# Kernel tuning notes

Measured on AMD Instinct MI355X. Metric: run time of the kernel, lower is better.

The kernel has to match this reference:

```python
import jax, jax.numpy as jnp
import numpy as np

E = 512       # token_size
H = 8         # num_heads
DH = E // H   # head dim
S = 16        # sequence_len (steps)
B = 128       # batch
MAX_SEQ = 64  # max_seq_len
IN = 256      # input_size
OUT = 128     # output_sz
NL = 2        # num_layers
MEM = E * MAX_SEQ + 1  # memory_size (last slot stores cur_idx)
EPS = 1e-5
NEG = -1e9


def _ln(x, s, b):
    mu = x.mean(-1, keepdims=True)
    var = ((x - mu) ** 2).mean(-1, keepdims=True)
    return (x - mu) / jnp.sqrt(var + EPS) * s + b


def _mha(x, mask, w_in, b_in, w_out, b_out):
    # x: (B, L, E); mask: (B, 1, L, L) bool, True = masked (torch semantics)
    bsz, L, _ = x.shape
    qkv = x @ w_in.T + b_in                      # (B, L, 3E)
    q, k, v = jnp.split(qkv, 3, axis=-1)
    q = q.reshape(bsz, L, H, DH)
    k = k.reshape(bsz, L, H, DH)
    v = v.reshape(bsz, L, H, DH)
    scores = jnp.einsum('bqhd,bkhd->bhqk', q, k) / jnp.sqrt(jnp.asarray(DH, x.dtype))
    scores = jnp.where(mask, NEG, scores)
    attn = jax.nn.softmax(scores, axis=-1)
    out = jnp.einsum('bhqk,bkhd->bqhd', attn, v).reshape(bsz, L, E)
    return out @ w_out.T + b_out


def setup_inputs() -> dict:
    key = jax.random.key(0)
    ks = jax.random.split(key, 16)
    sc = 0.02
    return {
        'sequences': jax.random.normal(ks[0], (S, B, IN), jnp.float32),
        'h_state': jnp.zeros((1, B, MEM), jnp.float32),
        'Win': jax.random.normal(ks[1], (E, IN), jnp.float32) * sc,
        'b_in': jnp.zeros((E,), jnp.float32),
        'Wout': jax.random.normal(ks[2], (OUT, E), jnp.float32) * sc,
        'b_out': jnp.zeros((OUT,), jnp.float32),
        'in_proj_w': jax.random.normal(ks[3], (NL, 3 * E, E), jnp.float32) * sc,
        'in_proj_b': jnp.zeros((NL, 3 * E), jnp.float32),
        'attn_out_w': jax.random.normal(ks[4], (NL, E, E), jnp.float32) * sc,
        'attn_out_b': jnp.zeros((NL, E), jnp.float32),
        'ln1_scale': jnp.ones((NL, E), jnp.float32),
        'ln1_bias': jnp.zeros((NL, E), jnp.float32),
        'ln2_scale': jnp.ones((NL, E), jnp.float32),
        'ln2_bias': jnp.zeros((NL, E), jnp.float32),
        'ff_w': jax.random.normal(ks[5], (NL, E, E), jnp.float32) * sc,
        'ff_b': jnp.zeros((NL, E), jnp.float32),
    }


def reference(sequences, h_state, Win, b_in, Wout, b_out, in_proj_w, in_proj_b,
              attn_out_w, attn_out_b, ln1_scale, ln1_bias, ln2_scale, ln2_bias,
              ff_w, ff_b):
    x = sequences @ Win.T + b_in                 # (S, B, E)
    h0 = h_state[0]
    cur_idx = h0[:, -1].astype(jnp.int32)        # (B,), zeros at rollout start
    hbuf = h0[:, :-1].reshape(B, MAX_SEQ, E)
    # fresh memory (cur_idx == 0) => max_len_here = S, static
    pad = hbuf[:, S:, :]
    h = hbuf[:, :S, :]
    pos = jnp.arange(S)
    bidx = jnp.arange(B)

    def step(carry, x_t):
        h, ci = carry
        h = h.at[bidx, ci].set(x_t)              # slot scatter write
        invalid = pos[None, :] > ci[:, None]     # (B, S)
        mask = invalid[:, None, :] | invalid[:, :, None]
        mask = mask & (pos != 0)[None, None, :]  # column 0 always attendable
        mask = mask[:, None, :, :]               # broadcast over heads
        for l in range(NL):
            attn = _mha(h, mask, in_proj_w[l], in_proj_b[l], attn_out_w[l], attn_out_b[l])
            h = _ln(h + attn, ln1_scale[l], ln1_bias[l])
            h = _ln(h + h @ ff_w[l].T + ff_b[l], ln2_scale[l], ln2_bias[l])
        out = h[bidx, ci] @ Wout.T + b_out       # (B, OUT)
        return (h, ci + 1), out

    (h_fin, ci_fin), outputs = jax.lax.scan(step, (h, cur_idx), x)
    new_h = jnp.concatenate([h_fin, pad], axis=1).reshape(B, MEM - 1)
    new_h = jnp.concatenate([new_h, ci_fin[:, None].astype(new_h.dtype)], axis=-1)[None]
    return outputs, new_h
```

## Files before the change

kernel.cpp:

```cpp
#include <hip/hip_runtime.h>

typedef __attribute__((ext_vector_type(8))) short short8;
typedef __attribute__((ext_vector_type(4))) float f32x4;
typedef __attribute__((ext_vector_type(4))) int int4v;
typedef unsigned short ushort_t;
typedef unsigned char u8;

#define E 512
#define SS 16
#define BB 128
#define IND 256
#define OUTD 128
#define MEMD 32769
#define NEGV -1000000000.0f
#define EPSV 1e-5f

#define MFMA  __builtin_amdgcn_mfma_f32_16x16x32_bf16
#define MFMAI8(a, b, c) __builtin_amdgcn_mfma_i32_16x16x64_i8((a), (b), (c), 0, 0, 0)

#define GLV(dst, base, off) \
  asm volatile("global_load_dwordx4 %0, %1, %2" : "=v"(dst) : "v"(off), "s"(base))
#define WVX_(x, n) asm volatile("s_waitcnt vmcnt(" #n ")" : "+v"(x))
#define WVX(x, n) WVX_(x, n)

__device__ __forceinline__ void bar_lds() {
  asm volatile("s_waitcnt lgkmcnt(0)\ns_barrier" ::: "memory");
}

__device__ __forceinline__ unsigned short f2bf(float f) {
  union { float f; unsigned int u; } v; v.f = f;
  unsigned int u = v.u;
  unsigned int r = u + 0x7fffu + ((u >> 16) & 1u);
  return (unsigned short)(r >> 16);
}
__device__ __forceinline__ float bf2f(unsigned short h) {
  union { unsigned int u; float f; } v; v.u = ((unsigned int)h) << 16;
  return v.f;
}
__device__ __forceinline__ int q8(float x) {
  return __float2int_rn(fminf(fmaxf(x, -127.f), 127.f));
}
__device__ __forceinline__ void quant8_store(u8* dst, const float* h) {
  int q[8];
#pragma unroll
  for (int j = 0; j < 8; ++j) q[j] = q8(h[j] * 32.f);
  unsigned int p0 = (q[0]&255) | ((q[1]&255)<<8) | ((q[2]&255)<<16) | ((q[3]&255)<<24);
  unsigned int p1 = (q[4]&255) | ((q[5]&255)<<8) | ((q[6]&255)<<16) | ((q[7]&255)<<24);
  *(unsigned int*)(dst)     = p0;
  *(unsigned int*)(dst + 4) = p1;
}

__global__ __launch_bounds__(256) void wscale_kernel(
    const float* __restrict__ ipw, const float* __restrict__ aow,
    const float* __restrict__ ffw, const float* __restrict__ wout,
    float* __restrict__ scl)
{
  int wv = blockIdx.x * 4 + (threadIdx.x >> 6);
  int lane = threadIdx.x & 63;
  const float* row;
  if (wv < 3072)      row = ipw  + (size_t)wv * 512;
  else if (wv < 4096) row = aow  + (size_t)(wv - 3072) * 512;
  else if (wv < 5120) row = ffw  + (size_t)(wv - 4096) * 512;
  else                row = wout + (size_t)(wv - 5120) * 512;
  float m = 0.f;
#pragma unroll
  for (int k = 0; k < 8; ++k) m = fmaxf(m, fabsf(row[lane + 64*k]));
  m = fmaxf(m, __shfl_xor(m, 1));
  m = fmaxf(m, __shfl_xor(m, 2));
  m = fmaxf(m, __shfl_xor(m, 4));
  m = fmaxf(m, __shfl_xor(m, 8));
  m = fmaxf(m, __shfl_xor(m, 16));
  m = fmaxf(m, __shfl_xor(m, 32));
  if (lane == 0) scl[wv] = (m > 0.f) ? m * (1.f / 127.f) : 1.f;
}

__device__ __forceinline__ void packmatI8(u8* __restrict__ dst, const float* __restrict__ src,
                                          const float* __restrict__ sclrow,
                                          int n, int tid, int stride) {
  for (int i = tid; i < n; i += stride) {
    int j = i & 15, lane = (i >> 4) & 63, kt = (i >> 10) & 7, T = i >> 13;
    int row = T * 16 + (lane & 15);
    int col = kt * 64 + ((lane >> 4) << 4) + j;
    float s = sclrow[row];
    int q = q8(src[(size_t)row * 512 + col] / s);
    dst[i] = (u8)(q & 0xff);
  }
}

__global__ __launch_bounds__(256) void wconvert_kernel(
    const float* __restrict__ ipw, const float* __restrict__ aow,
    const float* __restrict__ ffw, const float* __restrict__ wout,
    const float* __restrict__ win, const float* __restrict__ scl,
    u8* __restrict__ win8, u8* __restrict__ wo8,
    u8* __restrict__ wf8, u8* __restrict__ wout8,
    float* __restrict__ winT)
{
  const int tid = blockIdx.x * blockDim.x + threadIdx.x;
  const int stride = gridDim.x * blockDim.x;
  packmatI8(win8,  ipw,  scl,        2*1536*E, tid, stride);
  packmatI8(wo8,   aow,  scl + 3072, 2*E*E,    tid, stride);
  packmatI8(wf8,   ffw,  scl + 4096, 2*E*E,    tid, stride);
  packmatI8(wout8, wout, scl + 5120, OUTD*E,   tid, stride);
  for (int i = tid; i < E*IND; i += stride) {
    int o = i / IND, k = i % IND;
    winT[k*E + o] = win[i];
  }
}

__global__ __launch_bounds__(512) void xproj_kernel(
    const float* __restrict__ seq, const float* __restrict__ winT,
    const float* __restrict__ b_in, float* __restrict__ X)
{
  const int b = blockIdx.x;
  const int th = threadIdx.x;
  __shared__ float sq[SS * IND];
  for (int i = th; i < SS * IND; i += 512) {
    int t = i >> 8, k = i & 255;
    sq[i] = seq[((size_t)t * BB + b) * IND + k];
  }
  __syncthreads();
  float acc[SS];
#pragma unroll
  for (int t = 0; t < SS; ++t) acc[t] = 0.f;
  for (int k = 0; k < IND; ++k) {
    float w = winT[k * E + th];
#pragma unroll
    for (int t = 0; t < SS; ++t) acc[t] += sq[t * IND + k] * w;
  }
  float bias = b_in[th];
#pragma unroll
  for (int t = 0; t < SS; ++t)
    X[((size_t)t * BB + b) * E + th] = acc[t] + bias;
}

__global__ __launch_bounds__(1024, 4) void encoder_kernel(
    const float* __restrict__ Xpre, const float* __restrict__ hstate,
    const u8* __restrict__ win8, const u8* __restrict__ wo8,
    const u8* __restrict__ wf8, const u8* __restrict__ wout8,
    const float* __restrict__ scl,
    const float* __restrict__ ipb, const float* __restrict__ aob,
    const float* __restrict__ l1s, const float* __restrict__ l1b,
    const float* __restrict__ l2s, const float* __restrict__ l2b,
    const float* __restrict__ ffb, const float* __restrict__ bout,
    float* __restrict__ out)
{
  const int b = blockIdx.x;
  const int th = threadIdx.x;
  const int lane = th & 63;
  const int w = th >> 6;
  const int g = lane >> 4;
  const int c = lane & 15;
  const int fb = lane << 3;
  const int fq = w*16 + c;

  unsigned int vofs[8];
#pragma unroll
  for (int i = 0; i < 8; ++i)
    vofs[i] = (unsigned int)w * 8192u + (unsigned int)lane * 16u + (unsigned int)i * 1024u;

  __shared__ u8 h_i8[16*528];
  __shared__ ushort_t qk[9216];
  __shared__ ushort_t vbuf[10240];
  __shared__ ushort_t p_lds[2560];
  __shared__ ushort_t lnp[4096];

  ushort_t* q_lds = qk;
  ushort_t* k_lds = qk + 4608;
  u8* abuf_i8 = (u8*)qk;
  ushort_t* dbuf = qk;

  const size_t hsb = (size_t)b * MEMD;
  const int ci0 = (int)hstate[hsb + 32768];
  const float boutr = bout[(w&7)*16 + c];
  const float mw = scl[5120 + (w&7)*16 + c] * (1.f/32.f);

  float hreg[8];
  {
#pragma unroll
    for (int j = 0; j < 8; ++j) hreg[j] = hstate[hsb + (size_t)w*E + fb + j];
    quant8_store(h_i8 + w*528 + fb, hreg);
  }
  for (int i = th; i < 2560; i += 1024) p_lds[i] = 0;
  for (int i = th; i < 4096; i += 1024) {
    int h2 = i >> 10, dh = (i >> 4) & 63, t16 = i & 15;
    vbuf[h2*2560 + dh*40 + 16 + t16] = 0;
  }
  for (int i = th; i < 4096; i += 1024) {
    int l = i >> 11, arr = (i >> 9) & 3, idx = i & 511;
    float v = (arr == 0 ? l1s : arr == 1 ? l1b : arr == 2 ? l2s : l2b)[l*512 + idx];
    lnp[i] = f2bf(v);
  }
  bar_lds();

#pragma unroll 1
  for (int t = 0; t < SS; ++t) {
    const int cic = ci0 + t;
    if (cic < 16 && w == cic) {
#pragma unroll
      for (int j = 0; j < 8; ++j) hreg[j] = Xpre[((size_t)t*BB + b)*E + fb + j];
      quant8_store(h_i8 + w*528 + fb, hreg);
    }
    bar_lds();

#pragma unroll 1
    for (int l = 0; l < 2; ++l) {
      const float* bq_ = ipb + l*1536 + fq;
      const float biq0 = bq_[0],    biq1 = bq_[256];
      const float bik0 = bq_[512],  bik1 = bq_[768];
      const float biv0 = bq_[1024], biv1 = bq_[1280];
      const float aob0 = aob[l*512 + fq], aob1 = aob[l*512 + 256 + fq];
      const float ffb0 = ffb[l*512 + fq], ffb1 = ffb[l*512 + 256 + fq];
      const float* sip = scl + l*1536;
      const float mq0 = sip[fq]       * (1.f/32.f), mq1 = sip[256 + fq]  * (1.f/32.f);
      const float mk0 = sip[512 + fq] * (1.f/32.f), mk1 = sip[768 + fq]  * (1.f/32.f);
      const float mv0 = sip[1024+ fq] * (1.f/32.f), mv1 = sip[1280 + fq] * (1.f/32.f);
      const float* swo = scl + 3072 + l*512;
      const float mo0 = swo[fq] * (1.f/32.f), mo1 = swo[256 + fq] * (1.f/32.f);
      const float* swf = scl + 4096 + l*512;
      const float mf0 = swf[fq] * (1.f/32.f), mf1 = swf[256 + fq] * (1.f/32.f);

      const u8* wiL = win8 + (size_t)l*786432;
      const u8* woL = wo8 + (size_t)l*262144;
      const u8* wfL = wf8 + (size_t)l*262144;

      int4v oacc0 = {0,0,0,0}, oacc1 = oacc0;

#pragma unroll 1
      for (int pass = 0; pass < 2; ++pass) {
        const int hl = w >> 2;
        const int dhb = (w & 3) * 16;

        {
          const u8* A8 = h_i8 + c*528 + g*16;
          const u8* uq = wiL + (size_t)pass*131072;
          const u8* uk = uq + 262144;
          const u8* uv = uq + 524288;
          int4v aq = {0,0,0,0}, ak = aq, av = aq;
          int4v Bq[4], Bk[4], Bv[4];
          GLV(Bq[0], uq, vofs[0]); GLV(Bk[0], uk, vofs[0]); GLV(Bv[0], uv, vofs[0]);
          GLV(Bq[1], uq, vofs[1]); GLV(Bk[1], uk, vofs[1]); GLV(Bv[1], uv, vofs[1]);
          GLV(Bq[2], uq, vofs[2]); GLV(Bk[2], uk, vofs[2]); GLV(Bv[2], uv, vofs[2]);
          GLV(Bq[3], uq, vofs[3]); GLV(Bk[3], uk, vofs[3]); GLV(Bv[3], uv, vofs[3]);

#define QKV_STEP(kt2, nq, nk, nv) { \
            int4v a = *(const int4v*)(A8 + (kt2)*64); \
            WVX(Bq[(kt2)&3], nq); aq = MFMAI8(a, Bq[(kt2)&3], aq); \
            WVX(Bk[(kt2)&3], nk); ak = MFMAI8(a, Bk[(kt2)&3], ak); \
            WVX(Bv[(kt2)&3], nv); av = MFMAI8(a, Bv[(kt2)&3], av); \
            if ((kt2) < 4) { \
              GLV(Bq[(kt2)&3], uq, vofs[(kt2)+4]); \
              GLV(Bk[(kt2)&3], uk, vofs[(kt2)+4]); \
              GLV(Bv[(kt2)&3], uv, vofs[(kt2)+4]); \
            } }
          QKV_STEP(0, 11, 10, 9)
          QKV_STEP(1, 11, 10, 9)
          QKV_STEP(2, 11, 10, 9)
          QKV_STEP(3, 11, 10, 9)
          QKV_STEP(4, 11, 10, 9)
          QKV_STEP(5,  8,  7, 6)
          QKV_STEP(6,  5,  4, 3)
          QKV_STEP(7,  2,  1, 0)

          const float biq = pass ? biq1 : biq0;
          const float bik = pass ? bik1 : bik0;
          const float biv = pass ? biv1 : biv0;
          const float mq = pass ? mq1 : mq0;
          const float mk = pass ? mk1 : mk0;
          const float mv = pass ? mv1 : mv0;
#pragma unroll
          for (int r = 0; r < 4; ++r) {
            int tok = 4*g + r;
            q_lds[hl*1152 + tok*72 + dhb + c] = f2bf((float)aq[r]*mq + biq);
            k_lds[hl*1152 + tok*72 + dhb + c] = f2bf((float)ak[r]*mk + bik);
            vbuf[hl*2560 + (dhb + c)*40 + tok] = f2bf((float)av[r]*mv + biv);
          }
        }
        bar_lds();

        int4v O0[4], O1[4];
        {
          const u8* uo0 = woL + pass*4096;
          const u8* uo1 = uo0 + 131072;
          GLV(O0[0], uo0, vofs[0]); GLV(O1[0], uo1, vofs[0]);
          GLV(O0[1], uo0, vofs[1]); GLV(O1[1], uo1, vofs[1]);
          GLV(O0[2], uo0, vofs[2]); GLV(O1[2], uo1, vofs[2]);
          GLV(O0[3], uo0, vofs[3]); GLV(O1[3], uo1, vofs[3]);
        }

        if (w < 4) {
          f32x4 sc = {0.f,0.f,0.f,0.f};
#pragma unroll
          for (int k2 = 0; k2 < 2; ++k2) {
            short8 qa = *(const short8*)&q_lds[w*1152 + c*72 + k2*32 + g*8];
            short8 kb = *(const short8*)&k_lds[w*1152 + c*72 + k2*32 + g*8];
            sc = MFMA(qa, kb, sc, 0,0,0);
          }
          float sv[4], mx[4], ex[4], sm[4];
#pragma unroll
          for (int r = 0; r < 4; ++r) {
            int row = 4*g + r;
            bool msk = ((c > cic) || (row > cic)) && (c != 0);
            sv[r] = msk ? NEGV : sc[r]*0.125f;
            mx[r] = sv[r];
          }
#pragma unroll
          for (int r = 0; r < 4; ++r) {
            mx[r] = fmaxf(mx[r], __shfl_xor(mx[r], 1));
            mx[r] = fmaxf(mx[r], __shfl_xor(mx[r], 2));
            mx[r] = fmaxf(mx[r], __shfl_xor(mx[r], 4));
            mx[r] = fmaxf(mx[r], __shfl_xor(mx[r], 8));
          }
#pragma unroll
          for (int r = 0; r < 4; ++r) { ex[r] = __expf(sv[r] - mx[r]); sm[r] = ex[r]; }
#pragma unroll
          for (int r = 0; r < 4; ++r) {
            sm[r] += __shfl_xor(sm[r], 1);
            sm[r] += __shfl_xor(sm[r], 2);
            sm[r] += __shfl_xor(sm[r], 4);
            sm[r] += __shfl_xor(sm[r], 8);
          }
#pragma unroll
          for (int r = 0; r < 4; ++r)
            p_lds[w*640 + (4*g + r)*40 + c] = f2bf(ex[r] / sm[r]);
        }
        bar_lds();

        {
          const int hl2 = w >> 2, ct = w & 3;
          short8 pa = *(const short8*)&p_lds[hl2*640 + c*40 + g*8];
          short8 vb = *(const short8*)&vbuf[hl2*2560 + (ct*16 + c)*40 + g*8];
          f32x4 ov = {0.f,0.f,0.f,0.f};
          ov = MFMA(pa, vb, ov, 0,0,0);
#pragma unroll
          for (int r = 0; r < 4; ++r)
            abuf_i8[(4*g + r)*272 + hl2*64 + ct*16 + c] = (u8)(q8(ov[r]*32.f) & 0xff);
        }
        bar_lds();

        {
          const u8* A8o = abuf_i8 + c*272 + g*16;
#define OP_STEP(kt2, n0, n1) { \
            int4v a = *(const int4v*)(A8o + (kt2)*64); \
            WVX(O0[kt2], n0); oacc0 = MFMAI8(a, O0[kt2], oacc0); \
            WVX(O1[kt2], n1); oacc1 = MFMAI8(a, O1[kt2], oacc1); }
          OP_STEP(0, 7, 6)
          OP_STEP(1, 5, 4)
          OP_STEP(2, 3, 2)
          OP_STEP(3, 1, 0)
        }
        bar_lds();
      }

#pragma unroll
      for (int r = 0; r < 4; ++r) {
        dbuf[(4*g + r)*520 + fq]       = f2bf((float)oacc0[r]*mo0 + aob0);
        dbuf[(4*g + r)*520 + 256 + fq] = f2bf((float)oacc1[r]*mo1 + aob1);
      }
      bar_lds();

      int4v F0[4], F1[4];
      const u8* uf0 = wfL;
      const u8* uf1 = wfL + 131072;
      GLV(F0[0], uf0, vofs[0]); GLV(F1[0], uf1, vofs[0]);
      GLV(F0[1], uf0, vofs[1]); GLV(F1[1], uf1, vofs[1]);
      GLV(F0[2], uf0, vofs[2]); GLV(F1[2], uf1, vofs[2]);
      GLV(F0[3], uf0, vofs[3]); GLV(F1[3], uf1, vofs[3]);

      {
        const ushort_t* lpS = lnp + l*2048;
        const ushort_t* lpB = lnp + l*2048 + 512;
        float sum = 0.f;
#pragma unroll
        for (int j = 0; j < 8; ++j) {
          hreg[j] += bf2f(dbuf[w*520 + fb + j]);
          sum += hreg[j];
        }
        sum += __shfl_xor(sum, 1); sum += __shfl_xor(sum, 2); sum += __shfl_xor(sum, 4);
        sum += __shfl_xor(sum, 8); sum += __shfl_xor(sum, 16); sum += __shfl_xor(sum, 32);
        float mu = sum * (1.0f/512.0f);
        float s2 = 0.f;
#pragma unroll
        for (int j = 0; j < 8; ++j) { float dd = hreg[j] - mu; s2 += dd*dd; }
        s2 += __shfl_xor(s2, 1); s2 += __shfl_xor(s2, 2); s2 += __shfl_xor(s2, 4);
        s2 += __shfl_xor(s2, 8); s2 += __shfl_xor(s2, 16); s2 += __shfl_xor(s2, 32);
        float rs = rsqrtf(s2 * (1.0f/512.0f) + EPSV);
#pragma unroll
        for (int j = 0; j < 8; ++j)
          hreg[j] = (hreg[j] - mu) * rs * bf2f(lpS[fb + j]) + bf2f(lpB[fb + j]);
        quant8_store(h_i8 + w*528 + fb, hreg);
      }
      bar_lds();

      {
        int4v f0 = {0,0,0,0}, f1 = f0;
        const u8* A8 = h_i8 + c*528 + g*16;
#define FF_STEP(kt2, n0, n1) { \
          int4v a = *(const int4v*)(A8 + (kt2)*64); \
          WVX(F0[(kt2)&3], n0); f0 = MFMAI8(a, F0[(kt2)&3], f0); \
          WVX(F1[(kt2)&3], n1); f1 = MFMAI8(a, F1[(kt2)&3], f1); \
          if ((kt2) < 4) { \
            GLV(F0[(kt2)&3], uf0, vofs[(kt2)+4]); \
            GLV(F1[(kt2)&3], uf1, vofs[(kt2)+4]); \
          } }
        FF_STEP(0, 7, 6)
        FF_STEP(1, 7, 6)
        FF_STEP(2, 7, 6)
        FF_STEP(3, 7, 6)
        FF_STEP(4, 7, 6)
        FF_STEP(5, 5, 4)
        FF_STEP(6, 3, 2)
        FF_STEP(7, 1, 0)
        bar_lds();
#pragma unroll
        for (int r = 0; r < 4; ++r) {
          dbuf[(4*g + r)*520 + fq]       = f2bf((float)f0[r]*mf0 + ffb0);
          dbuf[(4*g + r)*520 + 256 + fq] = f2bf((float)f1[r]*mf1 + ffb1);
        }
      }
      bar_lds();

      {
        const ushort_t* lpS = lnp + l*2048 + 1024;
        const ushort_t* lpB = lnp + l*2048 + 1536;
        float sum = 0.f;
#pragma unroll
        for (int j = 0; j < 8; ++j) {
          hreg[j] += bf2f(dbuf[w*520 + fb + j]);
          sum += hreg[j];
        }
        sum += __shfl_xor(sum, 1); sum += __shfl_xor(sum, 2); sum += __shfl_xor(sum, 4);
        sum += __shfl_xor(sum, 8); sum += __shfl_xor(sum, 16); sum += __shfl_xor(sum, 32);
        float mu = sum * (1.0f/512.0f);
        float s2 = 0.f;
#pragma unroll
        for (int j = 0; j < 8; ++j) { float dd = hreg[j] - mu; s2 += dd*dd; }
        s2 += __shfl_xor(s2, 1); s2 += __shfl_xor(s2, 2); s2 += __shfl_xor(s2, 4);
        s2 += __shfl_xor(s2, 8); s2 += __shfl_xor(s2, 16); s2 += __shfl_xor(s2, 32);
        float rs = rsqrtf(s2 * (1.0f/512.0f) + EPSV);
#pragma unroll
        for (int j = 0; j < 8; ++j)
          hreg[j] = (hreg[j] - mu) * rs * bf2f(lpS[fb + j]) + bf2f(lpB[fb + j]);
        quant8_store(h_i8 + w*528 + fb, hreg);
      }
      bar_lds();
    }

    if (w < 8) {
      const int crow = (cic < 15) ? cic : 15;
      const u8* A8 = h_i8 + c*528 + g*16;
      int4v WB[8];
      GLV(WB[0], wout8, vofs[0]); GLV(WB[1], wout8, vofs[1]);
      GLV(WB[2], wout8, vofs[2]); GLV(WB[3], wout8, vofs[3]);
      GLV(WB[4], wout8, vofs[4]); GLV(WB[5], wout8, vofs[5]);
      GLV(WB[6], wout8, vofs[6]); GLV(WB[7], wout8, vofs[7]);
      int4v oo = {0,0,0,0};
#define WOUT_STEP(kt2, n) { \
        int4v a = *(const int4v*)(A8 + (kt2)*64); \
        WVX(WB[kt2], n); oo = MFMAI8(a, WB[kt2], oo); }
      WOUT_STEP(0, 7)
      WOUT_STEP(1, 6)
      WOUT_STEP(2, 5)
      WOUT_STEP(3, 4)
      WOUT_STEP(4, 3)
      WOUT_STEP(5, 2)
      WOUT_STEP(6, 1)
      WOUT_STEP(7, 0)
      if (g == (crow >> 2)) {
        int r = crow & 3;
        int val = (r == 0) ? oo[0] : (r == 1) ? oo[1] : (r == 2) ? oo[2] : oo[3];
        out[((size_t)t*BB + b)*OUTD + w*16 + c] = (float)val * mw + boutr;
      }
    }
    bar_lds();
  }

  const size_t OB = (size_t)SS * BB * OUTD;
#pragma unroll
  for (int j = 0; j < 8; ++j)
    out[OB + hsb + (size_t)w*E + fb + j] = hreg[j];
  for (int i = th; i < 48*512; i += 1024)
    out[OB + hsb + 8192 + i] = hstate[hsb + 8192 + i];
  if (th == 0) out[OB + hsb + 32768] = (float)(ci0 + SS);
}

extern "C" void kernel_launch(void* const* d_in, const int* in_sizes, int n_in,
                              void* d_out, int out_size, void* d_ws, size_t ws_size,
                              hipStream_t stream) {
  const float* seq  = (const float*)d_in[0];
  const float* hs   = (const float*)d_in[1];
  const float* Win  = (const float*)d_in[2];
  const float* b_in = (const float*)d_in[3];
  const float* Wout = (const float*)d_in[4];
  const float* bo   = (const float*)d_in[5];
  const float* ipw  = (const float*)d_in[6];
  const float* ipb  = (const float*)d_in[7];
  const float* aow  = (const float*)d_in[8];
  const float* aob  = (const float*)d_in[9];
  const float* l1s  = (const float*)d_in[10];
  const float* l1b  = (const float*)d_in[11];
  const float* l2s  = (const float*)d_in[12];
  const float* l2b  = (const float*)d_in[13];
  const float* ffw  = (const float*)d_in[14];
  const float* ffb  = (const float*)d_in[15];

  char* ws = (char*)d_ws;
  u8*    win8  = (u8*)   (ws + 0);
  u8*    wo8   = (u8*)   (ws + 1572864);
  u8*    wf8   = (u8*)   (ws + 2097152);
  u8*    wout8 = (u8*)   (ws + 2621440);
  float* scl   = (float*)(ws + 2686976);
  float* winT  = (float*)(ws + 2707968);
  float* X     = (float*)(ws + 3232256);

  wscale_kernel<<<1312, 256, 0, stream>>>(ipw, aow, ffw, Wout, scl);
  wconvert_kernel<<<512, 256, 0, stream>>>(ipw, aow, ffw, Wout, Win, scl,
                                           win8, wo8, wf8, wout8, winT);
  xproj_kernel<<<BB, 512, 0, stream>>>(seq, winT, b_in, X);
  encoder_kernel<<<BB, 1024, 0, stream>>>(X, hs, win8, wo8, wf8, wout8, scl,
                                          ipb, aob, l1s, l1b, l2s, l2b, ffb, bo,
                                          (float*)d_out);
}
```

Baseline: 785.3 us.

## Prefetch next QKV weight tiles across phases and fuse softmax with PV per wave

Hoists the first two QKV weight tile loads out of each pass, issuing them during the previous phase (after the out-projection, after the layer norm, after the output projection), so they overlap with earlier work and the stall at the start of each QKV GEMM shrinks. It also has all 16 waves compute the score and softmax tile redundantly into a private per-wave P buffer. That lets each wave feed its own PV MFMA directly, removing one block-wide barrier per pass. The cost is extra LDS (a larger P buffer and a separate attention-output buffer) and duplicated QK/softmax work. The vmcnt wait counts inside the existing macros must stay consistent with the loads now issued earlier.

```diff
diff --git a/kernel.cpp b/kernel.cpp
--- a/kernel.cpp
+++ b/kernel.cpp
@@ -161,12 +161,12 @@
   __shared__ u8 h_i8[16*528];
   __shared__ ushort_t qk[9216];
   __shared__ ushort_t vbuf[10240];
-  __shared__ ushort_t p_lds[2560];
+  __shared__ ushort_t p_w[9216];
+  __shared__ u8 abuf_i8[16*272];
   __shared__ ushort_t lnp[4096];
 
   ushort_t* q_lds = qk;
   ushort_t* k_lds = qk + 4608;
-  u8* abuf_i8 = (u8*)qk;
   ushort_t* dbuf = qk;
 
   const size_t hsb = (size_t)b * MEMD;
@@ -180,7 +180,7 @@
     for (int j = 0; j < 8; ++j) hreg[j] = hstate[hsb + (size_t)w*E + fb + j];
     quant8_store(h_i8 + w*528 + fb, hreg);
   }
-  for (int i = th; i < 2560; i += 1024) p_lds[i] = 0;
+  for (int i = th; i < 9216; i += 1024) p_w[i] = 0;
   for (int i = th; i < 4096; i += 1024) {
     int h2 = i >> 10, dh = (i >> 4) & 63, t16 = i & 15;
     vbuf[h2*2560 + dh*40 + 16 + t16] = 0;
@@ -191,6 +191,14 @@
     lnp[i] = f2bf(v);
   }
   bar_lds();
+
+  int4v Bq[4], Bk[4], Bv[4];
+
+  {
+    const u8* uq = win8;
+    GLV(Bq[0], uq, vofs[0]); GLV(Bk[0], uq + 262144, vofs[0]); GLV(Bv[0], uq + 524288, vofs[0]);
+    GLV(Bq[1], uq, vofs[1]); GLV(Bk[1], uq + 262144, vofs[1]); GLV(Bv[1], uq + 524288, vofs[1]);
+  }
 
 #pragma unroll 1
   for (int t = 0; t < SS; ++t) {
@@ -236,9 +244,6 @@
           const u8* uk = uq + 262144;
           const u8* uv = uq + 524288;
           int4v aq = {0,0,0,0}, ak = aq, av = aq;
-          int4v Bq[4], Bk[4], Bv[4];
-          GLV(Bq[0], uq, vofs[0]); GLV(Bk[0], uk, vofs[0]); GLV(Bv[0], uv, vofs[0]);
-          GLV(Bq[1], uq, vofs[1]); GLV(Bk[1], uk, vofs[1]); GLV(Bv[1], uv, vofs[1]);
           GLV(Bq[2], uq, vofs[2]); GLV(Bk[2], uk, vofs[2]); GLV(Bv[2], uv, vofs[2]);
           GLV(Bq[3], uq, vofs[3]); GLV(Bk[3], uk, vofs[3]); GLV(Bv[3], uv, vofs[3]);
 
@@ -287,12 +292,13 @@
           GLV(O0[3], uo0, vofs[3]); GLV(O1[3], uo1, vofs[3]);
         }
 
-        if (w < 4) {
+        {
+          const int hl2 = w >> 2, ct = w & 3;
           f32x4 sc = {0.f,0.f,0.f,0.f};
 #pragma unroll
           for (int k2 = 0; k2 < 2; ++k2) {
-            short8 qa = *(const short8*)&q_lds[w*1152 + c*72 + k2*32 + g*8];
-            short8 kb = *(const short8*)&k_lds[w*1152 + c*72 + k2*32 + g*8];
+            short8 qa = *(const short8*)&q_lds[hl2*1152 + c*72 + k2*32 + g*8];
+            short8 kb = *(const short8*)&k_lds[hl2*1152 + c*72 + k2*32 + g*8];
             sc = MFMA(qa, kb, sc, 0,0,0);
           }
           float sv[4], mx[4], ex[4], sm[4];
@@ -319,15 +325,11 @@
             sm[r] += __shfl_xor(sm[r], 4);
             sm[r] += __shfl_xor(sm[r], 8);
           }
+          ushort_t* pw = p_w + w*576;
 #pragma unroll
           for (int r = 0; r < 4; ++r)
-            p_lds[w*640 + (4*g + r)*40 + c] = f2bf(ex[r] / sm[r]);
-        }
-        bar_lds();
-
-        {
-          const int hl2 = w >> 2, ct = w & 3;
-          short8 pa = *(const short8*)&p_lds[hl2*640 + c*40 + g*8];
+            pw[(4*g + r)*36 + c] = f2bf(ex[r] / sm[r]);
+          short8 pa = *(const short8*)&pw[c*36 + g*8];
           short8 vb = *(const short8*)&vbuf[hl2*2560 + (ct*16 + c)*40 + g*8];
           f32x4 ov = {0.f,0.f,0.f,0.f};
           ov = MFMA(pa, vb, ov, 0,0,0);
@@ -347,6 +349,11 @@
           OP_STEP(1, 5, 4)
           OP_STEP(2, 3, 2)
           OP_STEP(3, 1, 0)
+          if (pass == 0) {
+            const u8* nq = wiL + 131072;
+            GLV(Bq[0], nq, vofs[0]); GLV(Bk[0], nq + 262144, vofs[0]); GLV(Bv[0], nq + 524288, vofs[0]);
+            GLV(Bq[1], nq, vofs[1]); GLV(Bk[1], nq + 262144, vofs[1]); GLV(Bv[1], nq + 524288, vofs[1]);
+          }
         }
         bar_lds();
       }
@@ -441,6 +448,11 @@
         for (int j = 0; j < 8; ++j)
           hreg[j] = (hreg[j] - mu) * rs * bf2f(lpS[fb + j]) + bf2f(lpB[fb + j]);
         quant8_store(h_i8 + w*528 + fb, hreg);
+      }
+      if (l == 0) {
+        const u8* nq = win8 + 786432;
+        GLV(Bq[0], nq, vofs[0]); GLV(Bk[0], nq + 262144, vofs[0]); GLV(Bv[0], nq + 524288, vofs[0]);
+        GLV(Bq[1], nq, vofs[1]); GLV(Bk[1], nq + 262144, vofs[1]); GLV(Bv[1], nq + 524288, vofs[1]);
       }
       bar_lds();
     }
@@ -471,9 +483,15 @@
         out[((size_t)t*BB + b)*OUTD + w*16 + c] = (float)val * mw + boutr;
       }
     }
+    {
+      const u8* nq = win8;
+      GLV(Bq[0], nq, vofs[0]); GLV(Bk[0], nq + 262144, vofs[0]); GLV(Bv[0], nq + 524288, vofs[0]);
+      GLV(Bq[1], nq, vofs[1]); GLV(Bk[1], nq + 262144, vofs[1]); GLV(Bv[1], nq + 524288, vofs[1]);
+    }
     bar_lds();
   }
 
+  asm volatile("s_waitcnt vmcnt(0)" ::: "memory");
   const size_t OB = (size_t)SS * BB * OUTD;
 #pragma unroll
   for (int j = 0; j < 8; ++j)
```

Measured after the change: 936.8 us. 1.19x slower.
